# Performance work log

Measured on AMD Instinct MI355X. Metric: run time of the kernel, lower is better.

## Reference

```python
import jax, jax.numpy as jnp
import numpy as np

N_ANCHORS = 262144
N_GT = 100
IMG = 1024.0
N_SAMPLE = 256
POS_RATIO = 0.5
POS_T = 0.7
NEG_T = 0.3
ALLOWED_BORDER = 0.0
NUM_FG = int(POS_RATIO * N_SAMPLE)  # 128


def compute_overlap(a, g):
    """IoU between anchors a:(N,4) and gt g:(R,4), py-faster-rcnn +1 pixel convention."""
    area_a = (a[:, 2] - a[:, 0] + 1.0) * (a[:, 3] - a[:, 1] + 1.0)          # (N,)
    area_g = (g[:, 2] - g[:, 0] + 1.0) * (g[:, 3] - g[:, 1] + 1.0)          # (R,)
    iw = jnp.minimum(a[:, None, 2], g[None, :, 2]) - jnp.maximum(a[:, None, 0], g[None, :, 0]) + 1.0
    ih = jnp.minimum(a[:, None, 3], g[None, :, 3]) - jnp.maximum(a[:, None, 1], g[None, :, 1]) + 1.0
    inter = jnp.maximum(iw, 0.0) * jnp.maximum(ih, 0.0)                     # (N,R)
    return inter / (area_a[:, None] + area_g[None, :] - inter)


def bbox_transform(gt, an):
    """Encode gt boxes relative to anchors -> (dx,dy,dw,dh), shape (N,4)."""
    aw = an[:, 2] - an[:, 0] + 1.0
    ah = an[:, 3] - an[:, 1] + 1.0
    acx = an[:, 0] + 0.5 * aw
    acy = an[:, 1] + 0.5 * ah
    gw = gt[:, 2] - gt[:, 0] + 1.0
    gh = gt[:, 3] - gt[:, 1] + 1.0
    gcx = gt[:, 0] + 0.5 * gw
    gcy = gt[:, 1] + 0.5 * gh
    return jnp.stack([(gcx - acx) / aw, (gcy - acy) / ah,
                      jnp.log(gw / aw), jnp.log(gh / ah)], axis=1)


def keep_at_most(mask, k, key):
    """Keep at most k True entries of mask, chosen uniformly at random (fixed shape)."""
    r = jnp.where(mask, jax.random.uniform(key, mask.shape), jnp.inf)
    rank = jnp.argsort(jnp.argsort(r))  # rank[i] = position of i in ascending sort
    return mask & (rank < k)


def anchor_target(anchors, image_shape, gt, key):
    # anchors: (N,4), gt: (R,4)
    R = gt.shape[0]
    inside = ((anchors[:, 0] >= -ALLOWED_BORDER) & (anchors[:, 1] >= -ALLOWED_BORDER)
              & (anchors[:, 2] < ALLOWED_BORDER + image_shape[1])
              & (anchors[:, 3] < ALLOWED_BORDER + image_shape[0]))            # (N,)
    iou = compute_overlap(anchors, gt)                                        # (N,R)
    iou_m = jnp.where(inside[:, None], iou, -1.0)  # restrict to inside anchors
    max_ov = jnp.max(iou_m, axis=1)                                           # (N,)

    k1, k2, k3 = jax.random.split(key, 3)
    labels = jnp.full(anchors.shape[:1], -1.0, dtype=jnp.float32)
    # clobber_positives=False: background first
    labels = jnp.where(inside & (max_ov < NEG_T), 0.0, labels)
    # per-gt argmax anchors (tie set), randomly truncated to at most R like tf.random_shuffle[:R]
    gt_max = jnp.max(iou_m, axis=0)                                           # (R,)
    cand = jnp.any(iou_m == gt_max[None, :], axis=1) & inside                 # (N,)
    cand = keep_at_most(cand, R, k1)
    labels = jnp.where(cand, 1.0, labels)
    labels = jnp.where(inside & (max_ov >= POS_T), 1.0, labels)

    # balance: subsample positives to NUM_FG
    fg = labels == 1.0
    labels = jnp.where(fg & ~keep_at_most(fg, NUM_FG, k2), -1.0, labels)
    # subsample negatives to n_sample - n_fg
    n_fg = jnp.sum(labels == 1.0)
    bg = labels == 0.0
    labels = jnp.where(bg & ~keep_at_most(bg, N_SAMPLE - n_fg, k3), -1.0, labels)
    # umap: outside anchors stay -1
    labels = jnp.where(inside, labels, -1.0)

    # bbox targets: faithful to original tf.gather(gt, to_int32(max_overlaps))
    idx = jnp.clip(max_ov.astype(jnp.int32), 0, R - 1)
    tgt = bbox_transform(gt[idx], anchors)                                    # (N,4)
    tgt = jnp.where(inside[:, None], tgt, 0.0)  # scatter_nd at inside indices
    return labels[None], tgt[None]


def setup_inputs() -> dict:
    key = jax.random.key(0)
    k1, k2, k3, k4 = jax.random.split(key, 4)
    ctr = jax.random.uniform(k1, (N_ANCHORS, 2), minval=-64.0, maxval=IMG + 64.0)
    wh = jax.random.uniform(k2, (N_ANCHORS, 2), minval=16.0, maxval=256.0)
    anchors = jnp.concatenate([ctr - 0.5 * wh, ctr + 0.5 * wh], axis=1)
    gctr = jax.random.uniform(k3, (N_GT, 2), minval=100.0, maxval=IMG - 100.0)
    gwh = jax.random.uniform(k4, (N_GT, 2), minval=30.0, maxval=200.0)
    gt = jnp.concatenate([gctr - 0.5 * gwh, gctr + 0.5 * gwh], axis=1)
    return {"total_anchors": anchors[None],
            "image_shape": jnp.array([IMG, IMG], jnp.float32),
            "gt_boxes": gt[None]}


def reference(total_anchors, image_shape, gt_boxes):
    key = jax.random.key(42)  # original uses unseeded tf.random_shuffle
    labels, bbox_reg_targets = anchor_target(total_anchors[0], image_shape,
                                             gt_boxes[0][:, :4], key)
    return labels, bbox_reg_targets
```

## Files before the change

### kernel.cpp

```cpp
#include <hip/hip_runtime.h>
#include <stdint.h>

#define NGT_MAX 128
#define CAND_CAP 8192
#define RANK_CAP 2048
#define FILT_CAP 16384
#define SUB_CAP 2048


__host__ __device__ inline void tf2x32(uint32_t k0, uint32_t k1, uint32_t c0, uint32_t c1,
                                       uint32_t& o0, uint32_t& o1) {
  uint32_t ks[3] = {k0, k1, k0 ^ k1 ^ 0x1BD11BDAu};
  uint32_t x0 = c0 + ks[0];
  uint32_t x1 = c1 + ks[1];
  const int rot[2][4] = {{13, 15, 26, 6}, {17, 29, 16, 24}};
#pragma unroll
  for (int i = 0; i < 5; ++i) {
#pragma unroll
    for (int j = 0; j < 4; ++j) {
      x0 += x1;
      int r = rot[i & 1][j];
      x1 = (x1 << r) | (x1 >> (32 - r));
      x1 ^= x0;
    }
    x0 += ks[(i + 1) % 3];
    x1 += ks[(i + 2) % 3] + (uint32_t)(i + 1);
  }
  o0 = x0; o1 = x1;
}

__device__ inline uint64_t sel_key(uint32_t i, uint32_t ka, uint32_t kb) {
  uint32_t o0, o1;
  tf2x32(ka, kb, 0u, i, o0, o1);
  uint32_t bits = o0 ^ o1;
  return ((uint64_t)(bits >> 9) << 32) | (uint64_t)i;
}

__device__ inline uint32_t fmap(float v) {
  uint32_t u = __float_as_uint(v);
  return (u & 0x80000000u) ? ~u : (u | 0x80000000u);
}
__device__ inline float funmap(uint32_t m) {
  return (m & 0x80000000u) ? __uint_as_float(m & 0x7FFFFFFFu) : __uint_as_float(~m);
}

__global__ void __launch_bounds__(256)
k_main(const float4* __restrict__ anc, const float* __restrict__ img,
       const float4* __restrict__ gt, int N, int R, int bOff,
       uint32_t* __restrict__ pmax, uint32_t* __restrict__ gmaxu,
       float* __restrict__ LBL, float4* __restrict__ TGT,
       uint32_t* __restrict__ pmeta) {
  __shared__ float4 sgt[NGT_MAX];
  __shared__ float sarea[NGT_MAX];
  __shared__ float sq[64 * 101];
  __shared__ uint32_t scnt[2];
  const int t = threadIdx.x;
  const int b = blockIdx.x + bOff;
  if (t < 2) scnt[t] = 0u;
  if (t < R) {
    float4 g = gt[t];
    sgt[t] = g;
    {
#pragma clang fp contract(off)
      sarea[t] = (g.z - g.x + 1.0f) * (g.w - g.y + 1.0f);
    }
  }
  __syncthreads();
  const int lane = t & 63, lm = t & 3, q = t >> 2;
  const int i = b * 256 + t;
  const float H = img[0], W = img[1];
  float4 a = anc[i];
  bool inside = (a.x >= 0.0f) && (a.y >= 0.0f) && (a.z < W) && (a.w < H);
  float area_a;
  {
#pragma clang fp contract(off)
    area_a = (a.z - a.x + 1.0f) * (a.w - a.y + 1.0f);
  }
  if (!inside) area_a = __uint_as_float(0x7FC00000u);
  const bool b1 = (lm == 1), b2 = (lm == 2), b3 = (lm == 3);
  float part[25];
  float vmax = -1.0f;
#pragma unroll
  for (int s = 0; s < 25; ++s) {
    const int gb0 = 4 * s;
    if (gb0 >= R) break;
    float v2q[4];
#pragma unroll
    for (int k = 0; k < 4; ++k) {
      const int g = gb0 + k;
      if (g < R) {
        float4 gb = sgt[g];
        float v;
        {
#pragma clang fp contract(off)
          float iw = fminf(a.z, gb.z) - fmaxf(a.x, gb.x) + 1.0f;
          float ih = fminf(a.w, gb.w) - fmaxf(a.y, gb.y) + 1.0f;
          float inter = fmaxf(iw, 0.0f) * fmaxf(ih, 0.0f);
          v = inter / (area_a + sarea[g] - inter);
        }
        vmax = fmaxf(vmax, v);
        int s1 = __builtin_amdgcn_mov_dpp(__float_as_int(v), 0xB1, 0xF, 0xF, true);
        float v1 = fmaxf(v, __int_as_float(s1));
        int s2 = __builtin_amdgcn_mov_dpp(__float_as_int(v1), 0x4E, 0xF, 0xF, true);
        v2q[k] = fmaxf(v1, __int_as_float(s2));
      } else {
        v2q[k] = -1.0f;
      }
    }
    float p = v2q[0];
    p = b1 ? v2q[1] : p;
    p = b2 ? v2q[2] : p;
    p = b3 ? v2q[3] : p;
    part[s] = p;
  }
  float lbl = -1.0f;
  if (inside) {
    if (vmax < 0.3f) lbl = 0.0f;
    if (vmax >= 0.7f) lbl = 1.0f;
  }
  LBL[i] = lbl;
  unsigned long long bf = __ballot(lbl == 1.0f);
  unsigned long long bb = __ballot(lbl == 0.0f);
  if (lane == 0) {
    atomicAdd(&scnt[0], (uint32_t)__popcll(bf));
    atomicAdd(&scnt[1], (uint32_t)__popcll(bb));
  }
  float4 o = make_float4(0.f, 0.f, 0.f, 0.f);
  if (inside) {
    int idx = (int)vmax;
    idx = idx < 0 ? 0 : idx;
    idx = idx > R - 1 ? R - 1 : idx;
    float4 gb = sgt[idx];
    {
#pragma clang fp contract(off)
      float aw = a.z - a.x + 1.0f;
      float ah = a.w - a.y + 1.0f;
      float acx = a.x + 0.5f * aw;
      float acy = a.y + 0.5f * ah;
      float gw = gb.z - gb.x + 1.0f;
      float gh = gb.w - gb.y + 1.0f;
      float gcx = gb.x + 0.5f * gw;
      float gcy = gb.y + 0.5f * gh;
      o.x = (gcx - acx) / aw;
      o.y = (gcy - acy) / ah;
      o.z = logf(gw / aw);
      o.w = logf(gh / ah);
    }
  }
  TGT[i] = o;
#pragma unroll
  for (int s = 0; s < 25; ++s) {
    const int g = 4 * s + lm;
    if (4 * s >= R) break;
    if (g < R) sq[q * 101 + g] = part[s];
  }
  __syncthreads();
  if (t < R) {
    float m = -1.0f;
#pragma unroll 8
    for (int k2 = 0; k2 < 64; ++k2) m = fmaxf(m, sq[k2 * 101 + t]);
    uint32_t u = fmap(m);
    pmax[b * R + t] = u;
    if (u > gmaxu[t]) atomicMax(&gmaxu[t], u);
  }
  if (t == 0) pmeta[b] = scnt[0] | (scnt[1] << 16);
}

__global__ void __launch_bounds__(256)
k_cand(const float4* __restrict__ anc, const float* __restrict__ img,
       const float4* __restrict__ gt, int N, int R,
       const uint32_t* __restrict__ pmax, const uint32_t* __restrict__ gmaxu,
       const float* __restrict__ LBL,
       uint64_t* __restrict__ candList, uint32_t* __restrict__ candLbl,
       uint32_t* __restrict__ counters, uint32_t ka, uint32_t kb) {
  __shared__ int tg[NGT_MAX];
  __shared__ float tgm[NGT_MAX];
  __shared__ uint64_t buf[256];
  __shared__ uint32_t bufL[256];
  __shared__ uint32_t bcnt, bbase;
  __shared__ int tcnt;
  const int t = threadIdx.x, b = blockIdx.x;
  if (t == 0) { tcnt = 0; bcnt = 0u; }
  __syncthreads();
  if (t < R) {
    uint32_t pm = pmax[b * R + t];
    uint32_t gm = gmaxu[t];
    if (pm == gm) { int p = atomicAdd(&tcnt, 1); tg[p] = t; tgm[p] = funmap(gm); }
  }
  __syncthreads();
  const int C0 = tcnt;
  if (C0 == 0) return;
  const int i = b * 256 + t;
  const float H = img[0], W = img[1];
  float4 a = anc[i];
  bool inside = (a.x >= 0.0f) && (a.y >= 0.0f) && (a.z < W) && (a.w < H);
  if (inside) {
    float area_a;
    {
#pragma clang fp contract(off)
      area_a = (a.z - a.x + 1.0f) * (a.w - a.y + 1.0f);
    }
    bool cand = false;
    for (int j = 0; j < C0; ++j) {
      float4 gb = gt[tg[j]];
      float v;
      {
#pragma clang fp contract(off)
        float ag = (gb.z - gb.x + 1.0f) * (gb.w - gb.y + 1.0f);
        float iw = fminf(a.z, gb.z) - fmaxf(a.x, gb.x) + 1.0f;
        float ih = fminf(a.w, gb.w) - fmaxf(a.y, gb.y) + 1.0f;
        float inter = fmaxf(iw, 0.0f) * fmaxf(ih, 0.0f);
        v = inter / (area_a + ag - inter);
      }
      cand = cand || (v == tgm[j]);
    }
    if (cand) {
      float old = LBL[i];
      uint32_t code = (old == 1.0f) ? 2u : ((old == 0.0f) ? 1u : 0u);
      uint32_t p = atomicAdd(&bcnt, 1u);
      buf[p] = sel_key((uint32_t)i, ka, kb);
      bufL[p] = code;
    }
  }
  __syncthreads();
  if (t == 0 && bcnt) bbase = atomicAdd(&counters[0], bcnt);
  __syncthreads();
  for (uint32_t j = t; j < bcnt; j += 256) {
    uint32_t p = bbase + j;
    if (p < CAND_CAP) { candList[p] = buf[j]; candLbl[p] = bufL[j]; }
  }
}

__global__ void __launch_bounds__(256)
k_gather(float* __restrict__ LBL, int N, int NB, int R,
         const uint64_t* __restrict__ candList, const uint32_t* __restrict__ candLbl,
         const uint32_t* __restrict__ pmeta,
         uint64_t* __restrict__ listF, uint64_t* __restrict__ listB,
         uint32_t* __restrict__ counters,
         uint32_t k2a, uint32_t k2b, uint32_t k3a, uint32_t k3b) {
  __shared__ uint64_t sub[RANK_CAP];
  __shared__ uint64_t red[256];
  __shared__ uint64_t bufF[256], bufB[256];
  __shared__ uint32_t sflag[256];
  __shared__ uint32_t sdFB[2];
  __shared__ uint32_t smeta[6];
  __shared__ uint32_t cF, cB, oF, oB;
  const int t = threadIdx.x, b = blockIdx.x;
  sflag[t] = 0u;
  if (t < 2) sdFB[t] = 0u;
  if (t == 0) { cF = 0u; cB = 0u; }
  uint64_t sm = 0;
  for (int j = t; j < NB; j += 256) {
    uint32_t v = pmeta[j];
    sm += (uint64_t)(v & 0xFFFFu) | ((uint64_t)(v >> 16) << 32);
  }
  red[t] = sm;
  uint32_t C = counters[0];
  if (C > RANK_CAP) C = RANK_CAP;
  __syncthreads();
  for (int s = 128; s > 0; s >>= 1) {
    if (t < s) red[t] += red[t + s];
    __syncthreads();
  }
  const uint32_t baseF = (uint32_t)(red[0] & 0xFFFFFFFFu);
  const uint32_t baseB = (uint32_t)(red[0] >> 32);
  for (uint32_t s = t; s < C; s += 256) sub[s] = candList[s];
  __syncthreads();
  for (uint32_t e = t; e < C; e += 256) {
    uint64_t key = sub[e];
    bool keep = true;
    if (C > (uint32_t)R) {
      uint32_t rank = 0;
      for (uint32_t j = 0; j < C; ++j) rank += (sub[j] < key) ? 1u : 0u;
      keep = (rank < (uint32_t)R);
    }
    if (keep) {
      uint32_t code = candLbl[e];
      if (code != 2u) atomicAdd(&sdFB[0], 1u);
      if (code == 1u) atomicAdd(&sdFB[1], 1u);
      uint32_t idx = (uint32_t)key;
      if ((int)(idx >> 8) == b) sflag[idx & 255u] = 1u;
    }
  }
  __syncthreads();
  if (t == 0) {
    uint32_t M1 = baseF + sdFB[0];
    uint32_t M2 = baseB - sdFB[1];
    uint32_t nfg = M1 < 128u ? M1 : 128u;
    uint32_t kbg = 256u - nfg;
    uint32_t needF = (M1 > 128u) ? 1u : 0u;
    uint32_t needB = (M2 > kbg) ? 1u : 0u;
    uint64_t Tf = 0, Tb = 0;
    if (needF) {
      Tf = (((uint64_t)(128u * 32u)) << 23) / (uint64_t)M1;
      if (Tf > (1u << 23)) Tf = (1u << 23);
    }
    if (needB) {
      Tb = (((uint64_t)(kbg * 32u)) << 23) / (uint64_t)M2;
      if (Tb > (1u << 23)) Tb = (1u << 23);
    }
    smeta[0] = needF; smeta[1] = needB; smeta[2] = (uint32_t)Tf; smeta[3] = (uint32_t)Tb;
    smeta[4] = M1; smeta[5] = M2;
    if (b == 0) {
      counters[1] = M1; counters[2] = M2;
      counters[8] = needF; counters[9] = needB;
      counters[10] = (uint32_t)Tf; counters[11] = (uint32_t)Tb;
      counters[12] = kbg;
    }
  }
  __syncthreads();
  const uint32_t needF = smeta[0], needB = smeta[1], Tf = smeta[2], Tb = smeta[3];
  const int i = b * 256 + t;
  float old = LBL[i];
  float l1 = sflag[t] ? 1.0f : old;
  float out = l1;
  if (l1 == 1.0f) {
    if (needF) {
      uint64_t key = sel_key((uint32_t)i, k2a, k2b);
      if ((uint32_t)(key >> 32) >= Tf) {
        out = -1.0f;
      } else {
        uint32_t p = atomicAdd(&cF, 1u);
        bufF[p] = key;
      }
    }
  } else if (l1 == 0.0f) {
    if (needB) {
      uint64_t key = sel_key((uint32_t)i, k3a, k3b);
      if ((uint32_t)(key >> 32) >= Tb) {
        out = -1.0f;
      } else {
        uint32_t p = atomicAdd(&cB, 1u);
        bufB[p] = key;
      }
    }
  }
  LBL[i] = out;
  __syncthreads();
  if (t == 0 && cF) oF = atomicAdd(&counters[4], cF);
  if (t == 64 && cB) oB = atomicAdd(&counters[5], cB);
  __syncthreads();
  for (uint32_t j = t; j < cF; j += 256) {
    uint32_t p = oF + j;
    if (p < FILT_CAP) listF[p] = bufF[j];
  }
  for (uint32_t j = t; j < cB; j += 256) {
    uint32_t p = oB + j;
    if (p < FILT_CAP) listB[p] = bufB[j];
  }
}

__device__ __forceinline__ void do_select(const uint64_t* list, uint32_t Mf, uint32_t k,
                                          uint32_t T, float* LBL, uint32_t* h,
                                          uint32_t* c0, uint32_t* c1, uint64_t* sub,
                                          uint32_t* scal) {
  const int t = threadIdx.x;
  if (Mf <= k) return;
  int bl = (T > 1u) ? (32 - __clz(T - 1u)) : 0;
  int shift = bl > 8 ? bl - 8 : 0;
  h[t] = 0u;
  if (t == 0) { scal[0] = 0u; scal[1] = 0u; scal[2] = 0u; }
  __syncthreads();
  for (uint32_t j = t; j < Mf; j += 256)
    atomicAdd(&h[((uint32_t)(list[j] >> 32)) >> shift], 1u);
  __syncthreads();
  c0[t] = h[t];
  __syncthreads();
  uint32_t* s = c0;
  uint32_t* d = c1;
  for (int dd = 1; dd < 256; dd <<= 1) {
    uint32_t v = s[t];
    if (t >= dd) v += s[t - dd];
    d[t] = v;
    __syncthreads();
    uint32_t* tmp = s; s = d; d = tmp;
  }
  uint32_t inc = s[t];
  uint32_t exc = inc - h[t];
  if (exc < k && inc >= k) { scal[1] = (uint32_t)t; scal[2] = k - exc; }
  __syncthreads();
  const uint32_t binb = scal[1], rneed = scal[2];
  for (uint32_t j = t; j < Mf; j += 256) {
    uint64_t key = list[j];
    uint32_t bin = ((uint32_t)(key >> 32)) >> shift;
    if (bin > binb) {
      LBL[(uint32_t)key] = -1.0f;
    } else if (bin == binb) {
      uint32_t p = atomicAdd(&scal[0], 1u);
      if (p < SUB_CAP) sub[p] = key;
    }
  }
  __syncthreads();
  uint32_t c = scal[0] < SUB_CAP ? scal[0] : SUB_CAP;
  for (uint32_t s2 = t; s2 < c; s2 += 256) {
    uint64_t key = sub[s2];
    uint32_t rank = 0u;
    for (uint32_t j = 0; j < c; ++j) rank += (sub[j] < key) ? 1u : 0u;
    if (rank >= rneed) LBL[(uint32_t)key] = -1.0f;
  }
  __syncthreads();
}

__global__ void __launch_bounds__(256)
k_sel(float* __restrict__ LBL, const uint64_t* __restrict__ listF,
      const uint64_t* __restrict__ listB, uint32_t* __restrict__ counters) {
  __shared__ uint32_t h[256], c0[256], c1[256];
  __shared__ uint64_t sub[SUB_CAP];
  __shared__ uint32_t scal[4];
  if (counters[8]) {
    uint32_t Mf = counters[4];
    if (Mf > FILT_CAP) Mf = FILT_CAP;
    do_select(listF, Mf, 128u, counters[10], LBL, h, c0, c1, sub, scal);
  }
  if (counters[9]) {
    uint32_t Mf = counters[5];
    if (Mf > FILT_CAP) Mf = FILT_CAP;
    do_select(listB, Mf, counters[12], counters[11], LBL, h, c0, c1, sub, scal);
  }
}

extern "C" void kernel_launch(void* const* d_in, const int* in_sizes, int n_in,
                              void* d_out, int out_size, void* d_ws, size_t ws_size,
                              hipStream_t stream) {
  (void)n_in; (void)out_size; (void)ws_size;
  const int N = in_sizes[0] / 4;
  const int R = in_sizes[2] / 4;
  const int NB = N / 256;
  const float4* anc = (const float4*)d_in[0];
  const float* img = (const float*)d_in[1];
  const float4* gtb = (const float4*)d_in[2];
  float* LBL = (float*)d_out;
  float4* TGT = (float4*)((float*)d_out + N);

  uint8_t* ws = (uint8_t*)d_ws;
  uint32_t* counters = (uint32_t*)ws;
  uint32_t* gmaxu = (uint32_t*)(ws + 512);
  uint32_t* pmeta = (uint32_t*)(ws + 1024);
  uint32_t* candLbl = (uint32_t*)(ws + 1024 + 4096);
  uint32_t* pmax = (uint32_t*)(ws + 65536);
  size_t off = 65536 + (size_t)NB * R * 4;
  off = (off + 7) & ~(size_t)7;
  uint64_t* candList = (uint64_t*)(ws + off);
  uint64_t* listF = (uint64_t*)(ws + off + CAND_CAP * 8);
  uint64_t* listB = (uint64_t*)(ws + off + CAND_CAP * 8 + FILT_CAP * 8);

  uint32_t k1a, k1b, k2a, k2b, k3a, k3b;
  tf2x32(0u, 42u, 0u, 0u, k1a, k1b);
  tf2x32(0u, 42u, 0u, 1u, k2a, k2b);
  tf2x32(0u, 42u, 0u, 2u, k3a, k3b);

  hipMemsetAsync(ws, 0, 1024, stream);
  k_main<<<NB / 2, 256, 0, stream>>>(anc, img, gtb, N, R, 0, pmax, gmaxu, LBL, TGT, pmeta);
  k_main<<<NB / 2, 256, 0, stream>>>(anc, img, gtb, N, R, NB / 2, pmax, gmaxu, LBL, TGT,
                                     pmeta);
  k_cand<<<NB, 256, 0, stream>>>(anc, img, gtb, N, R, pmax, gmaxu, LBL, candList, candLbl,
                                 counters, k1a, k1b);
  k_gather<<<NB, 256, 0, stream>>>(LBL, N, NB, R, candList, candLbl, pmeta, listF, listB,
                                   counters, k2a, k2b, k3a, k3b);
  k_sel<<<1, 256, 0, stream>>>(LBL, listF, listB, counters);
}
```

Baseline: 153.3 us.

## Replace quad-partial IoU column max with full-wave DPP reduction per GT

The per-GT column max over anchors in a block is now computed with a full 64-lane DPP wave reduction plus readlane for each GT box. This replaces the old scheme of 4-lane quad partials kept in 25 registers and reduced through a 64x101 shared-memory tile. Shared memory use and register pressure drop sharply, which may raise occupancy. The cost is more DPP and readlane instructions per GT, up to six shuffle steps instead of two. The two half-grid launches of the main kernel are also merged into one launch.

```diff
diff --git a/kernel.cpp b/kernel.cpp
--- a/kernel.cpp
+++ b/kernel.cpp
@@ -44,18 +44,35 @@
   return (m & 0x80000000u) ? __uint_as_float(m & 0x7FFFFFFFu) : __uint_as_float(~m);
 }
 
+__device__ inline float wave_max_dpp(float v) {
+  int x;
+  x = __builtin_amdgcn_mov_dpp(__float_as_int(v), 0xB1, 0xF, 0xF, true);
+  v = fmaxf(v, __int_as_float(x));
+  x = __builtin_amdgcn_mov_dpp(__float_as_int(v), 0x4E, 0xF, 0xF, true);
+  v = fmaxf(v, __int_as_float(x));
+  x = __builtin_amdgcn_mov_dpp(__float_as_int(v), 0x114, 0xF, 0xF, true);
+  v = fmaxf(v, __int_as_float(x));
+  x = __builtin_amdgcn_mov_dpp(__float_as_int(v), 0x118, 0xF, 0xF, true);
+  v = fmaxf(v, __int_as_float(x));
+  x = __builtin_amdgcn_mov_dpp(__float_as_int(v), 0x142, 0xF, 0xF, true);
+  v = fmaxf(v, __int_as_float(x));
+  x = __builtin_amdgcn_mov_dpp(__float_as_int(v), 0x143, 0xF, 0xF, true);
+  v = fmaxf(v, __int_as_float(x));
+  return v;
+}
+
 __global__ void __launch_bounds__(256)
 k_main(const float4* __restrict__ anc, const float* __restrict__ img,
-       const float4* __restrict__ gt, int N, int R, int bOff,
+       const float4* __restrict__ gt, int N, int R,
        uint32_t* __restrict__ pmax, uint32_t* __restrict__ gmaxu,
        float* __restrict__ LBL, float4* __restrict__ TGT,
        uint32_t* __restrict__ pmeta) {
   __shared__ float4 sgt[NGT_MAX];
   __shared__ float sarea[NGT_MAX];
-  __shared__ float sq[64 * 101];
+  __shared__ float swv[4 * 104];
   __shared__ uint32_t scnt[2];
   const int t = threadIdx.x;
-  const int b = blockIdx.x + bOff;
+  const int b = blockIdx.x;
   if (t < 2) scnt[t] = 0u;
   if (t < R) {
     float4 g = gt[t];
@@ -66,7 +83,7 @@
     }
   }
   __syncthreads();
-  const int lane = t & 63, lm = t & 3, q = t >> 2;
+  const int lane = t & 63, wid = t >> 6;
   const int i = b * 256 + t;
   const float H = img[0], W = img[1];
   float4 a = anc[i];
@@ -77,41 +94,23 @@
     area_a = (a.z - a.x + 1.0f) * (a.w - a.y + 1.0f);
   }
   if (!inside) area_a = __uint_as_float(0x7FC00000u);
-  const bool b1 = (lm == 1), b2 = (lm == 2), b3 = (lm == 3);
-  float part[25];
+  float part2[2] = {-1.0f, -1.0f};
   float vmax = -1.0f;
-#pragma unroll
-  for (int s = 0; s < 25; ++s) {
-    const int gb0 = 4 * s;
-    if (gb0 >= R) break;
-    float v2q[4];
-#pragma unroll
-    for (int k = 0; k < 4; ++k) {
-      const int g = gb0 + k;
-      if (g < R) {
-        float4 gb = sgt[g];
-        float v;
-        {
-#pragma clang fp contract(off)
-          float iw = fminf(a.z, gb.z) - fmaxf(a.x, gb.x) + 1.0f;
-          float ih = fminf(a.w, gb.w) - fmaxf(a.y, gb.y) + 1.0f;
-          float inter = fmaxf(iw, 0.0f) * fmaxf(ih, 0.0f);
-          v = inter / (area_a + sarea[g] - inter);
-        }
-        vmax = fmaxf(vmax, v);
-        int s1 = __builtin_amdgcn_mov_dpp(__float_as_int(v), 0xB1, 0xF, 0xF, true);
-        float v1 = fmaxf(v, __int_as_float(s1));
-        int s2 = __builtin_amdgcn_mov_dpp(__float_as_int(v1), 0x4E, 0xF, 0xF, true);
-        v2q[k] = fmaxf(v1, __int_as_float(s2));
-      } else {
-        v2q[k] = -1.0f;
-      }
-    }
-    float p = v2q[0];
-    p = b1 ? v2q[1] : p;
-    p = b2 ? v2q[2] : p;
-    p = b3 ? v2q[3] : p;
-    part[s] = p;
+#pragma unroll 4
+  for (int g = 0; g < R; ++g) {
+    float4 gb = sgt[g];
+    float v;
+    {
+#pragma clang fp contract(off)
+      float iw = fminf(a.z, gb.z) - fmaxf(a.x, gb.x) + 1.0f;
+      float ih = fminf(a.w, gb.w) - fmaxf(a.y, gb.y) + 1.0f;
+      float inter = fmaxf(iw, 0.0f) * fmaxf(ih, 0.0f);
+      v = inter / (area_a + sarea[g] - inter);
+    }
+    vmax = fmaxf(vmax, v);
+    float wm = wave_max_dpp(v);
+    float rl = __int_as_float(__builtin_amdgcn_readlane(__float_as_int(wm), 63));
+    if (lane == (g & 63)) part2[g >> 6] = rl;
   }
   float lbl = -1.0f;
   if (inside) {
@@ -148,17 +147,11 @@
     }
   }
   TGT[i] = o;
-#pragma unroll
-  for (int s = 0; s < 25; ++s) {
-    const int g = 4 * s + lm;
-    if (4 * s >= R) break;
-    if (g < R) sq[q * 101 + g] = part[s];
-  }
+  if (lane < R) swv[wid * 104 + lane] = part2[0];
+  if (64 + lane < R) swv[wid * 104 + 64 + lane] = part2[1];
   __syncthreads();
   if (t < R) {
-    float m = -1.0f;
-#pragma unroll 8
-    for (int k2 = 0; k2 < 64; ++k2) m = fmaxf(m, sq[k2 * 101 + t]);
+    float m = fmaxf(fmaxf(swv[t], swv[104 + t]), fmaxf(swv[208 + t], swv[312 + t]));
     uint32_t u = fmap(m);
     pmax[b * R + t] = u;
     if (u > gmaxu[t]) atomicMax(&gmaxu[t], u);
@@ -300,7 +293,6 @@
       if (Tb > (1u << 23)) Tb = (1u << 23);
     }
     smeta[0] = needF; smeta[1] = needB; smeta[2] = (uint32_t)Tf; smeta[3] = (uint32_t)Tb;
-    smeta[4] = M1; smeta[5] = M2;
     if (b == 0) {
       counters[1] = M1; counters[2] = M2;
       counters[8] = needF; counters[9] = needB;
@@ -450,9 +442,7 @@
   tf2x32(0u, 42u, 0u, 2u, k3a, k3b);
 
   hipMemsetAsync(ws, 0, 1024, stream);
-  k_main<<<NB / 2, 256, 0, stream>>>(anc, img, gtb, N, R, 0, pmax, gmaxu, LBL, TGT, pmeta);
-  k_main<<<NB / 2, 256, 0, stream>>>(anc, img, gtb, N, R, NB / 2, pmax, gmaxu, LBL, TGT,
-                                     pmeta);
+  k_main<<<NB, 256, 0, stream>>>(anc, img, gtb, N, R, pmax, gmaxu, LBL, TGT, pmeta);
   k_cand<<<NB, 256, 0, stream>>>(anc, img, gtb, N, R, pmax, gmaxu, LBL, candList, candLbl,
                                  counters, k1a, k1b);
   k_gather<<<NB, 256, 0, stream>>>(LBL, N, NB, R, candList, candLbl, pmeta, listF, listB,
```

New measurement: 143.5 us. 6.4% less time.

## Process two anchors per thread and halve per-block GT max partials

Applied to the files above, without the earlier changes.

k_main now has each thread compute IoU for two anchors, 512 per block, and folds both into one DPP-reduced partial per GT. This halves the per-block shared-memory max reduction and the pmax traffic, and replaces the two half-grid launches with one. k_cand and k_gather are adjusted to the 512-anchor block granularity. The per-GT loop drops its R bounds checks and assumes 100 GT boxes, which raises register pressure and relies on the fixed problem size.

```diff
diff --git a/kernel.cpp b/kernel.cpp
--- a/kernel.cpp
+++ b/kernel.cpp
@@ -44,9 +44,31 @@
   return (m & 0x80000000u) ? __uint_as_float(m & 0x7FFFFFFFu) : __uint_as_float(~m);
 }
 
+__device__ __forceinline__ float iou_ref(const float4& a, float area_a, const float4& gb,
+                                         float area_g) {
+#pragma clang fp contract(off)
+  float iw = fminf(a.z, gb.z) - fmaxf(a.x, gb.x) + 1.0f;
+  float ih = fminf(a.w, gb.w) - fmaxf(a.y, gb.y) + 1.0f;
+  float inter = fmaxf(iw, 0.0f) * fmaxf(ih, 0.0f);
+  return inter / (area_a + area_g - inter);
+}
+
+__device__ __forceinline__ float4 tgt_ref(const float4& a, const float4& gb) {
+#pragma clang fp contract(off)
+  float aw = a.z - a.x + 1.0f;
+  float ah = a.w - a.y + 1.0f;
+  float acx = a.x + 0.5f * aw;
+  float acy = a.y + 0.5f * ah;
+  float gw = gb.z - gb.x + 1.0f;
+  float gh = gb.w - gb.y + 1.0f;
+  float gcx = gb.x + 0.5f * gw;
+  float gcy = gb.y + 0.5f * gh;
+  return make_float4((gcx - acx) / aw, (gcy - acy) / ah, logf(gw / aw), logf(gh / ah));
+}
+
 __global__ void __launch_bounds__(256)
 k_main(const float4* __restrict__ anc, const float* __restrict__ img,
-       const float4* __restrict__ gt, int N, int R, int bOff,
+       const float4* __restrict__ gt, int N, int R,
        uint32_t* __restrict__ pmax, uint32_t* __restrict__ gmaxu,
        float* __restrict__ LBL, float4* __restrict__ TGT,
        uint32_t* __restrict__ pmeta) {
@@ -54,8 +76,7 @@
   __shared__ float sarea[NGT_MAX];
   __shared__ float sq[64 * 101];
   __shared__ uint32_t scnt[2];
-  const int t = threadIdx.x;
-  const int b = blockIdx.x + bOff;
+  const int t = threadIdx.x, b = blockIdx.x;
   if (t < 2) scnt[t] = 0u;
   if (t < R) {
     float4 g = gt[t];
@@ -67,45 +88,40 @@
   }
   __syncthreads();
   const int lane = t & 63, lm = t & 3, q = t >> 2;
-  const int i = b * 256 + t;
+  const int iA = b * 512 + t, iB = iA + 256;
   const float H = img[0], W = img[1];
-  float4 a = anc[i];
-  bool inside = (a.x >= 0.0f) && (a.y >= 0.0f) && (a.z < W) && (a.w < H);
-  float area_a;
+  float4 aA = anc[iA], aB = anc[iB];
+  bool inA = (aA.x >= 0.0f) && (aA.y >= 0.0f) && (aA.z < W) && (aA.w < H);
+  bool inB = (aB.x >= 0.0f) && (aB.y >= 0.0f) && (aB.z < W) && (aB.w < H);
+  float arA, arB;
   {
 #pragma clang fp contract(off)
-    area_a = (a.z - a.x + 1.0f) * (a.w - a.y + 1.0f);
-  }
-  if (!inside) area_a = __uint_as_float(0x7FC00000u);
+    arA = (aA.z - aA.x + 1.0f) * (aA.w - aA.y + 1.0f);
+    arB = (aB.z - aB.x + 1.0f) * (aB.w - aB.y + 1.0f);
+  }
+  if (!inA) arA = __uint_as_float(0x7FC00000u);
+  if (!inB) arB = __uint_as_float(0x7FC00000u);
   const bool b1 = (lm == 1), b2 = (lm == 2), b3 = (lm == 3);
   float part[25];
-  float vmax = -1.0f;
-#pragma unroll
+  float vmaxA = -1.0f, vmaxB = -1.0f;
+#pragma unroll 4
   for (int s = 0; s < 25; ++s) {
-    const int gb0 = 4 * s;
-    if (gb0 >= R) break;
     float v2q[4];
 #pragma unroll
     for (int k = 0; k < 4; ++k) {
-      const int g = gb0 + k;
-      if (g < R) {
-        float4 gb = sgt[g];
-        float v;
-        {
-#pragma clang fp contract(off)
-          float iw = fminf(a.z, gb.z) - fmaxf(a.x, gb.x) + 1.0f;
-          float ih = fminf(a.w, gb.w) - fmaxf(a.y, gb.y) + 1.0f;
-          float inter = fmaxf(iw, 0.0f) * fmaxf(ih, 0.0f);
-          v = inter / (area_a + sarea[g] - inter);
-        }
-        vmax = fmaxf(vmax, v);
-        int s1 = __builtin_amdgcn_mov_dpp(__float_as_int(v), 0xB1, 0xF, 0xF, true);
-        float v1 = fmaxf(v, __int_as_float(s1));
-        int s2 = __builtin_amdgcn_mov_dpp(__float_as_int(v1), 0x4E, 0xF, 0xF, true);
-        v2q[k] = fmaxf(v1, __int_as_float(s2));
-      } else {
-        v2q[k] = -1.0f;
-      }
+      const int g = 4 * s + k;
+      float4 gb = sgt[g];
+      float ag = sarea[g];
+      float vA = iou_ref(aA, arA, gb, ag);
+      float vB = iou_ref(aB, arB, gb, ag);
+      vmaxA = fmaxf(vmaxA, vA);
+      vmaxB = fmaxf(vmaxB, vB);
+      float vq = fmaxf(vA, vB);
+      int d1 = __builtin_amdgcn_mov_dpp(__float_as_int(vq), 0xB1, 0xF, 0xF, true);
+      vq = fmaxf(vq, __int_as_float(d1));
+      int d2 = __builtin_amdgcn_mov_dpp(__float_as_int(vq), 0x4E, 0xF, 0xF, true);
+      vq = fmaxf(vq, __int_as_float(d2));
+      v2q[k] = vq;
     }
     float p = v2q[0];
     p = b1 ? v2q[1] : p;
@@ -113,45 +129,35 @@
     p = b3 ? v2q[3] : p;
     part[s] = p;
   }
-  float lbl = -1.0f;
-  if (inside) {
-    if (vmax < 0.3f) lbl = 0.0f;
-    if (vmax >= 0.7f) lbl = 1.0f;
-  }
-  LBL[i] = lbl;
-  unsigned long long bf = __ballot(lbl == 1.0f);
-  unsigned long long bb = __ballot(lbl == 0.0f);
+  float lblA = -1.0f, lblB = -1.0f;
+  if (inA) { if (vmaxA < 0.3f) lblA = 0.0f; if (vmaxA >= 0.7f) lblA = 1.0f; }
+  if (inB) { if (vmaxB < 0.3f) lblB = 0.0f; if (vmaxB >= 0.7f) lblB = 1.0f; }
+  LBL[iA] = lblA;
+  LBL[iB] = lblB;
+  unsigned long long bf = __ballot(lblA == 1.0f);
+  unsigned long long bb = __ballot(lblA == 0.0f);
+  unsigned long long bf2 = __ballot(lblB == 1.0f);
+  unsigned long long bb2 = __ballot(lblB == 0.0f);
   if (lane == 0) {
-    atomicAdd(&scnt[0], (uint32_t)__popcll(bf));
-    atomicAdd(&scnt[1], (uint32_t)__popcll(bb));
-  }
-  float4 o = make_float4(0.f, 0.f, 0.f, 0.f);
-  if (inside) {
-    int idx = (int)vmax;
-    idx = idx < 0 ? 0 : idx;
-    idx = idx > R - 1 ? R - 1 : idx;
-    float4 gb = sgt[idx];
-    {
-#pragma clang fp contract(off)
-      float aw = a.z - a.x + 1.0f;
-      float ah = a.w - a.y + 1.0f;
-      float acx = a.x + 0.5f * aw;
-      float acy = a.y + 0.5f * ah;
-      float gw = gb.z - gb.x + 1.0f;
-      float gh = gb.w - gb.y + 1.0f;
-      float gcx = gb.x + 0.5f * gw;
-      float gcy = gb.y + 0.5f * gh;
-      o.x = (gcx - acx) / aw;
-      o.y = (gcy - acy) / ah;
-      o.z = logf(gw / aw);
-      o.w = logf(gh / ah);
-    }
-  }
-  TGT[i] = o;
+    atomicAdd(&scnt[0], (uint32_t)(__popcll(bf) + __popcll(bf2)));
+    atomicAdd(&scnt[1], (uint32_t)(__popcll(bb) + __popcll(bb2)));
+  }
+  float4 oA = make_float4(0.f, 0.f, 0.f, 0.f), oB = oA;
+  if (inA) {
+    int idx = (int)vmaxA;
+    idx = idx < 0 ? 0 : (idx > R - 1 ? R - 1 : idx);
+    oA = tgt_ref(aA, sgt[idx]);
+  }
+  if (inB) {
+    int idx = (int)vmaxB;
+    idx = idx < 0 ? 0 : (idx > R - 1 ? R - 1 : idx);
+    oB = tgt_ref(aB, sgt[idx]);
+  }
+  TGT[iA] = oA;
+  TGT[iB] = oB;
 #pragma unroll
   for (int s = 0; s < 25; ++s) {
     const int g = 4 * s + lm;
-    if (4 * s >= R) break;
     if (g < R) sq[q * 101 + g] = part[s];
   }
   __syncthreads();
@@ -175,8 +181,8 @@
        uint32_t* __restrict__ counters, uint32_t ka, uint32_t kb) {
   __shared__ int tg[NGT_MAX];
   __shared__ float tgm[NGT_MAX];
-  __shared__ uint64_t buf[256];
-  __shared__ uint32_t bufL[256];
+  __shared__ uint64_t buf[512];
+  __shared__ uint32_t bufL[512];
   __shared__ uint32_t bcnt, bbase;
   __shared__ int tcnt;
   const int t = threadIdx.x, b = blockIdx.x;
@@ -190,36 +196,36 @@
   __syncthreads();
   const int C0 = tcnt;
   if (C0 == 0) return;
-  const int i = b * 256 + t;
   const float H = img[0], W = img[1];
-  float4 a = anc[i];
-  bool inside = (a.x >= 0.0f) && (a.y >= 0.0f) && (a.z < W) && (a.w < H);
-  if (inside) {
-    float area_a;
-    {
-#pragma clang fp contract(off)
-      area_a = (a.z - a.x + 1.0f) * (a.w - a.y + 1.0f);
-    }
-    bool cand = false;
-    for (int j = 0; j < C0; ++j) {
-      float4 gb = gt[tg[j]];
-      float v;
+#pragma unroll
+  for (int half = 0; half < 2; ++half) {
+    const int i = b * 512 + half * 256 + t;
+    float4 a = anc[i];
+    bool inside = (a.x >= 0.0f) && (a.y >= 0.0f) && (a.z < W) && (a.w < H);
+    if (inside) {
+      float area_a;
       {
 #pragma clang fp contract(off)
-        float ag = (gb.z - gb.x + 1.0f) * (gb.w - gb.y + 1.0f);
-        float iw = fminf(a.z, gb.z) - fmaxf(a.x, gb.x) + 1.0f;
-        float ih = fminf(a.w, gb.w) - fmaxf(a.y, gb.y) + 1.0f;
-        float inter = fmaxf(iw, 0.0f) * fmaxf(ih, 0.0f);
-        v = inter / (area_a + ag - inter);
+        area_a = (a.z - a.x + 1.0f) * (a.w - a.y + 1.0f);
       }
-      cand = cand || (v == tgm[j]);
-    }
-    if (cand) {
-      float old = LBL[i];
-      uint32_t code = (old == 1.0f) ? 2u : ((old == 0.0f) ? 1u : 0u);
-      uint32_t p = atomicAdd(&bcnt, 1u);
-      buf[p] = sel_key((uint32_t)i, ka, kb);
-      bufL[p] = code;
+      bool cand = false;
+      for (int j = 0; j < C0; ++j) {
+        float4 gb = gt[tg[j]];
+        float ag;
+        {
+#pragma clang fp contract(off)
+          ag = (gb.z - gb.x + 1.0f) * (gb.w - gb.y + 1.0f);
+        }
+        float v = iou_ref(a, area_a, gb, ag);
+        cand = cand || (v == tgm[j]);
+      }
+      if (cand) {
+        float old = LBL[i];
+        uint32_t code = (old == 1.0f) ? 2u : ((old == 0.0f) ? 1u : 0u);
+        uint32_t p = atomicAdd(&bcnt, 1u);
+        buf[p] = sel_key((uint32_t)i, ka, kb);
+        bufL[p] = code;
+      }
     }
   }
   __syncthreads();
@@ -232,7 +238,7 @@
 }
 
 __global__ void __launch_bounds__(256)
-k_gather(float* __restrict__ LBL, int N, int NB, int R,
+k_gather(float* __restrict__ LBL, int N, int NBm, int R,
          const uint64_t* __restrict__ candList, const uint32_t* __restrict__ candLbl,
          const uint32_t* __restrict__ pmeta,
          uint64_t* __restrict__ listF, uint64_t* __restrict__ listB,
@@ -250,7 +256,7 @@
   if (t < 2) sdFB[t] = 0u;
   if (t == 0) { cF = 0u; cB = 0u; }
   uint64_t sm = 0;
-  for (int j = t; j < NB; j += 256) {
+  for (int j = t; j < NBm; j += 256) {
     uint32_t v = pmeta[j];
     sm += (uint64_t)(v & 0xFFFFu) | ((uint64_t)(v >> 16) << 32);
   }
@@ -300,7 +306,6 @@
       if (Tb > (1u << 23)) Tb = (1u << 23);
     }
     smeta[0] = needF; smeta[1] = needB; smeta[2] = (uint32_t)Tf; smeta[3] = (uint32_t)Tb;
-    smeta[4] = M1; smeta[5] = M2;
     if (b == 0) {
       counters[1] = M1; counters[2] = M2;
       counters[8] = needF; counters[9] = needB;
@@ -425,7 +430,8 @@
   (void)n_in; (void)out_size; (void)ws_size;
   const int N = in_sizes[0] / 4;
   const int R = in_sizes[2] / 4;
-  const int NB = N / 256;
+  const int NBm = N / 512;
+  const int NBg = N / 256;
   const float4* anc = (const float4*)d_in[0];
   const float* img = (const float*)d_in[1];
   const float4* gtb = (const float4*)d_in[2];
@@ -438,7 +444,7 @@
   uint32_t* pmeta = (uint32_t*)(ws + 1024);
   uint32_t* candLbl = (uint32_t*)(ws + 1024 + 4096);
   uint32_t* pmax = (uint32_t*)(ws + 65536);
-  size_t off = 65536 + (size_t)NB * R * 4;
+  size_t off = 65536 + (size_t)NBm * R * 4;
   off = (off + 7) & ~(size_t)7;
   uint64_t* candList = (uint64_t*)(ws + off);
   uint64_t* listF = (uint64_t*)(ws + off + CAND_CAP * 8);
@@ -450,12 +456,10 @@
   tf2x32(0u, 42u, 0u, 2u, k3a, k3b);
 
   hipMemsetAsync(ws, 0, 1024, stream);
-  k_main<<<NB / 2, 256, 0, stream>>>(anc, img, gtb, N, R, 0, pmax, gmaxu, LBL, TGT, pmeta);
-  k_main<<<NB / 2, 256, 0, stream>>>(anc, img, gtb, N, R, NB / 2, pmax, gmaxu, LBL, TGT,
-                                     pmeta);
-  k_cand<<<NB, 256, 0, stream>>>(anc, img, gtb, N, R, pmax, gmaxu, LBL, candList, candLbl,
-                                 counters, k1a, k1b);
-  k_gather<<<NB, 256, 0, stream>>>(LBL, N, NB, R, candList, candLbl, pmeta, listF, listB,
-                                   counters, k2a, k2b, k3a, k3b);
+  k_main<<<NBm, 256, 0, stream>>>(anc, img, gtb, N, R, pmax, gmaxu, LBL, TGT, pmeta);
+  k_cand<<<NBm, 256, 0, stream>>>(anc, img, gtb, N, R, pmax, gmaxu, LBL, candList,
+                                  candLbl, counters, k1a, k1b);
+  k_gather<<<NBg, 256, 0, stream>>>(LBL, N, NBm, R, candList, candLbl, pmeta, listF,
+                                    listB, counters, k2a, k2b, k3a, k3b);
   k_sel<<<1, 256, 0, stream>>>(LBL, listF, listB, counters);
 }
```

After: 149.2 us. -2.7%, faster.
